# Performance work log

Hardware: AMD Instinct MI355X
Metric: run time of the kernel (lower is better)

The kernel has to match this reference:

```python
import jax, jax.numpy as jnp
import numpy as np

B, N = 64, 16384
EPS_RT = 1e-06  # recovery_time epsilon from the torch code


def _init_params(key):
    ks = jax.random.split(key, 10)
    s = 0.1
    p = {}
    # ContextEncoder: 4 -> 16 -> 8 -> 1 (hidden_dim=8, first layer hidden*2)
    p['ctx_W1'] = jax.random.normal(ks[0], (4, 16), jnp.float32) * s
    p['ctx_b1'] = jnp.zeros((16,), jnp.float32)
    p['ctx_W2'] = jax.random.normal(ks[1], (16, 8), jnp.float32) * s
    p['ctx_b2'] = jnp.zeros((8,), jnp.float32)
    p['ctx_W3'] = jax.random.normal(ks[2], (8, 1), jnp.float32) * s
    p['ctx_b3'] = jnp.zeros((1,), jnp.float32)
    # RiskPropagationNetwork: 4 -> 64 -> 32 -> 16 -> 1
    p['p_W1'] = jax.random.normal(ks[3], (4, 64), jnp.float32) * s
    p['p_b1'] = jnp.zeros((64,), jnp.float32)
    p['p_W2'] = jax.random.normal(ks[4], (64, 32), jnp.float32) * s
    p['p_b2'] = jnp.zeros((32,), jnp.float32)
    p['p_W3'] = jax.random.normal(ks[5], (32, 16), jnp.float32) * s
    p['p_b3'] = jnp.zeros((16,), jnp.float32)
    p['p_Wo'] = jax.random.normal(ks[6], (16, 1), jnp.float32) * s
    p['p_bo'] = jnp.zeros((1,), jnp.float32)
    # learned scalar risk-component weights
    p['w_threat'] = jnp.float32(0.4)
    p['w_impact'] = jnp.float32(0.3)
    p['w_vuln'] = jnp.float32(0.2)
    p['w_ctx'] = jnp.float32(0.1)
    return p


def setup_inputs() -> dict:
    key = jax.random.key(0)
    ks = jax.random.split(key, 12)
    inp = {
        'threat_predictions': jax.random.normal(ks[0], (B, N), jnp.float32),
        'criticality': jax.random.uniform(ks[1], (B, N), jnp.float32),
        'connectivity': jax.random.uniform(ks[2], (B, N), jnp.float32),
        'sensitivity': jax.random.uniform(ks[3], (B, N), jnp.float32),
        'business_value': jax.random.uniform(ks[4], (B, N), jnp.float32),
        'data_sensitivity': jax.random.uniform(ks[5], (B, N), jnp.float32),
        'compliance_requirements': jax.random.uniform(ks[6], (B, N), jnp.float32),
        'recovery_time': jax.random.uniform(ks[7], (B, N), jnp.float32),
        'severity': jax.random.uniform(ks[8], (B, N), jnp.float32) * 10.0,
    }
    inp.update(_init_params(ks[9]))
    return inp


def _forward(threat_predictions, criticality, connectivity, sensitivity,
             business_value, data_sensitivity, compliance_requirements,
             recovery_time, severity,
             ctx_W1, ctx_b1, ctx_W2, ctx_b2, ctx_W3, ctx_b3,
             p_W1, p_b1, p_W2, p_b2, p_W3, p_b3, p_Wo, p_bo,
             w_threat, w_impact, w_vuln, w_ctx):
    # --- risk components ---
    threat_risk = jax.nn.sigmoid(threat_predictions * 3.0)
    m = jnp.max(criticality)
    impact_risk = jnp.where(m > 0, criticality / jnp.maximum(m, 1e-12), criticality)
    vuln_risk = severity / 10.0
    # ContextEncoder: concat 4 context scalars -> MLP -> sigmoid
    ctx_in = jnp.stack([business_value, data_sensitivity, compliance_requirements,
                        1.0 / (recovery_time + EPS_RT)], axis=-1)  # [B,N,4]
    h = jax.nn.relu(ctx_in @ ctx_W1 + ctx_b1)
    h = jax.nn.relu(h @ ctx_W2 + ctx_b2)
    context_risk = jax.nn.sigmoid((h @ ctx_W3 + ctx_b3)[..., 0])
    # --- weighted combination with normalized learned weights ---
    total_w = w_threat + w_impact + w_vuln + w_ctx
    base_risk = (w_threat * threat_risk + w_impact * impact_risk
                 + w_vuln * vuln_risk + w_ctx * context_risk) / total_w
    # --- RiskPropagationNetwork (dropout is identity in eval) ---
    feats = jnp.stack([base_risk, criticality, connectivity, sensitivity], axis=-1)  # [B,N,4]
    x = jax.nn.relu(feats @ p_W1 + p_b1)
    x = jax.nn.relu(x @ p_W2 + p_b2)
    x = jax.nn.relu(x @ p_W3 + p_b3)
    return jax.nn.sigmoid((x @ p_Wo + p_bo)[..., 0])  # [B,N]


def reference(threat_predictions, criticality, connectivity, sensitivity,
              business_value, data_sensitivity, compliance_requirements,
              recovery_time, severity,
              ctx_W1, ctx_b1, ctx_W2, ctx_b2, ctx_W3, ctx_b3,
              p_W1, p_b1, p_W2, p_b2, p_W3, p_b3, p_Wo, p_bo,
              w_threat, w_impact, w_vuln, w_ctx):
    return _forward(threat_predictions, criticality, connectivity, sensitivity,
                    business_value, data_sensitivity, compliance_requirements,
                    recovery_time, severity,
                    ctx_W1, ctx_b1, ctx_W2, ctx_b2, ctx_W3, ctx_b3,
                    p_W1, p_b1, p_W2, p_b2, p_W3, p_b3, p_Wo, p_bo,
                    w_threat, w_impact, w_vuln, w_ctx)
```

## Files before the change

### kernel.cpp

```cpp
#include <hip/hip_runtime.h>
#include <hip/hip_bf16.h>

typedef short bf16x8 __attribute__((ext_vector_type(8)));
typedef float f32x4 __attribute__((ext_vector_type(4)));
typedef unsigned int uint;

#define TOTAL (64 * 16384)
#define ITERS 2
#define BLOCKS (TOTAL / (256 * ITERS))
#define MAXBLOCKS 256

__device__ __forceinline__ uint bf16rne(float x) {
    uint b = __float_as_uint(x);
    return (b + 0x7fffu + ((b >> 16) & 1u)) >> 16;
}
__device__ __forceinline__ short bf16s(float x) { return (short)bf16rne(x); }
__device__ __forceinline__ uint pk2(float lo, float hi) {
    __hip_bfloat162 h2 = __float22bfloat162_rn(make_float2(lo, hi));
    uint u;
    __builtin_memcpy(&u, &h2, sizeof(u));
    return u;
}
__device__ __forceinline__ float relu_(float x) { return fmaxf(x, 0.0f); }
__device__ __forceinline__ float fast_sigmoid(float x) {
    return __builtin_amdgcn_rcpf(1.0f + __expf(-x));
}
__device__ __forceinline__ float dot4r(f32x4 v, float4 w) {
    return fmaf(relu_(v[0]), w.x, fmaf(relu_(v[1]), w.y,
           fmaf(relu_(v[2]), w.z, relu_(v[3]) * w.w)));
}
__device__ __forceinline__ bf16x8 u4bf(uint4 u) {
    bf16x8 r;
    __builtin_memcpy(&r, &u, sizeof(r));
    return r;
}

__global__ __launch_bounds__(256) void crit_max_kernel(
        const float* __restrict__ crit, float* __restrict__ ws, int n4) {
    __shared__ float smax[4];
    const int tid = threadIdx.x;
    float m = 0.0f;
    const float4* c4 = (const float4*)crit;
    for (int i = blockIdx.x * 256 + tid; i < n4; i += gridDim.x * 256) {
        float4 v = c4[i];
        m = fmaxf(fmaxf(m, v.x), fmaxf(fmaxf(v.y, v.z), v.w));
    }
#pragma unroll
    for (int off = 32; off > 0; off >>= 1)
        m = fmaxf(m, __shfl_xor(m, off));
    if ((tid & 63) == 0) smax[tid >> 6] = m;
    __syncthreads();
    if (tid == 0)
        ws[blockIdx.x] = fmaxf(fmaxf(smax[0], smax[1]), fmaxf(smax[2], smax[3]));
}

__global__ __launch_bounds__(256, 3) void risk_mfma_kernel(
        const float* __restrict__ tp,   const float* __restrict__ crit,
        const float* __restrict__ conn, const float* __restrict__ sens,
        const float* __restrict__ bv,   const float* __restrict__ dsv,
        const float* __restrict__ comp, const float* __restrict__ rt,
        const float* __restrict__ sev,
        const float* __restrict__ ctxW1, const float* __restrict__ ctxb1,
        const float* __restrict__ ctxW2, const float* __restrict__ ctxb2,
        const float* __restrict__ ctxW3, const float* __restrict__ ctxb3,
        const float* __restrict__ pW1,  const float* __restrict__ pb1,
        const float* __restrict__ pW2,  const float* __restrict__ pb2,
        const float* __restrict__ pW3,  const float* __restrict__ pb3,
        const float* __restrict__ pWo,  const float* __restrict__ pbo,
        const float* __restrict__ w_threat, const float* __restrict__ w_impact,
        const float* __restrict__ w_vuln,   const float* __restrict__ w_ctx,
        const float* __restrict__ ws_part,
        float* __restrict__ out) {
    const int lane = threadIdx.x & 63;
    const int g    = lane >> 4;
    const int c    = lane & 15;

    const bf16x8 z8 = {0,0,0,0,0,0,0,0};
    const f32x4  z4 = {0.f,0.f,0.f,0.f};

    float m;
    {
        float4 pm4 = ((const float4*)ws_part)[lane];
        float pm = fmaxf(fmaxf(pm4.x, pm4.y), fmaxf(pm4.z, pm4.w));
#pragma unroll
        for (int off = 32; off > 0; off >>= 1)
            pm = fmaxf(pm, __shfl_xor(pm, off));
        m = pm;
    }

    const float wt  = w_threat[0], wi = w_impact[0], wv = w_vuln[0], wc = w_ctx[0];
    const float inv_tw = 1.0f / (wt + wi + wv + wc);
    const float imul = (m > 0.0f) ? 1.0f / fmaxf(m, 1e-12f) : 1.0f;
    const float wcn = wc * inv_tw;
    const float cb3 = ctxb3[0];
    const float pbo0 = pbo[0];

    bf16x8 cwAll = z8;
    cwAll[0] = bf16s(ctxW1[c]);
    cwAll[1] = bf16s(ctxW1[16 + c]);
    cwAll[2] = bf16s(ctxW1[32 + c]);
    cwAll[3] = bf16s(ctxW1[48 + c]);
    cwAll[4] = bf16s(ctxb1[c]);
    bf16x8 cw2All = z8;
    if (c < 8) {
#pragma unroll
        for (int i = 0; i < 4; ++i)
            cw2All[i] = bf16s(ctxW2[(4 * g + i) * 8 + c]);
    }
    bf16x8 w1All[4];
#pragma unroll
    for (int nt = 0; nt < 4; ++nt) {
        bf16x8 f = z8;
        f[0] = bf16s(pW1[nt * 16 + c]);
        f[4] = bf16s(pb1[nt * 16 + c]);
        f[5] = bf16s(pW1[64 + nt * 16 + c]);
        f[6] = bf16s(pW1[128 + nt * 16 + c]);
        f[7] = bf16s(pW1[192 + nt * 16 + c]);
        w1All[nt] = f;
    }
    bf16x8 w2A[2][2];
#pragma unroll
    for (int mt = 0; mt < 2; ++mt)
#pragma unroll
        for (int kf = 0; kf < 2; ++kf) {
            bf16x8 f;
#pragma unroll
            for (int i = 0; i < 4; ++i)
                f[i] = bf16s(pW2[(kf * 32 + 4 * g + i) * 32 + mt * 16 + c]);
#pragma unroll
            for (int i = 4; i < 8; ++i)
                f[i] = bf16s(pW2[(kf * 32 + 16 + 4 * g + (i - 4)) * 32 + mt * 16 + c]);
            w2A[mt][kf] = f;
        }
    bf16x8 w3A;
#pragma unroll
    for (int i = 0; i < 4; ++i) w3A[i] = bf16s(pW3[(4 * g + i) * 16 + c]);
#pragma unroll
    for (int i = 4; i < 8; ++i) w3A[i] = bf16s(pW3[(16 + 4 * g + (i - 4)) * 16 + c]);

    f32x4 b2i[2];
#pragma unroll
    for (int mt = 0; mt < 2; ++mt) {
        float4 t = ((const float4*)pb2)[mt * 4 + g];
        b2i[mt] = (f32x4){t.x, t.y, t.z, t.w};
    }
    float4 t3 = ((const float4*)pb3)[g];
    f32x4 b3i = (f32x4){t3.x, t3.y, t3.z, t3.w};
    f32x4 cb2i = z4;
    float4 cw3v = make_float4(0.f, 0.f, 0.f, 0.f);
    if (g < 2) {
        float4 tb = ((const float4*)ctxb2)[g];
        cb2i = (f32x4){tb.x, tb.y, tb.z, tb.w};
        cw3v = ((const float4*)ctxW3)[g];
    }
    float4 wog = ((const float4*)pWo)[g];

    const int eblock = blockIdx.x * (256 * ITERS);

#pragma unroll 1
    for (int it = 0; it < ITERS; ++it) {
        const int ewave = eblock + it * 256 + (int)(threadIdx.x >> 6) * 64;
        uint4 fv;
        float pbase;
        {
            const int e = ewave + lane;
            float tpv = tp[e], cv = crit[e], cnv = conn[e], snv = sens[e];
            float bvv = bv[e], dvv = dsv[e], cpv = comp[e], rtv = rt[e], svv = sev[e];
            float threat = fast_sigmoid(3.0f * tpv);
            float impact = cv * imul;
            float vuln   = svv * 0.1f;
            float invrt  = __builtin_amdgcn_rcpf(rtv + 1e-6f);
            pbase = (wt * threat + wi * impact + wv * vuln) * inv_tw;
            fv.x = pk2(bvv, dvv);
            fv.y = pk2(cpv, invrt);
            fv.z = pk2(1.0f, cv);
            fv.w = pk2(cnv, snv);
        }
        uint4 Bt[4];
#pragma unroll
        for (int t = 0; t < 4; ++t) {
            bool sel = (g == t);
            Bt[t].x = sel ? fv.x : 0u;
            Bt[t].y = sel ? fv.y : 0u;
            Bt[t].z = sel ? fv.z : 0u;
            Bt[t].w = sel ? fv.w : 0u;
        }
        float pcv[4];
#pragma unroll
        for (int t = 0; t < 4; ++t) {
            f32x4 cc1 = __builtin_amdgcn_mfma_f32_16x16x32_bf16(cwAll, u4bf(Bt[t]), z4, 0, 0, 0);
            uint4 bu;
            bu.x = pk2(relu_(cc1[0]), relu_(cc1[1]));
            bu.y = pk2(relu_(cc1[2]), relu_(cc1[3]));
            bu.z = 0u;
            bu.w = 0u;
            f32x4 cc2 = __builtin_amdgcn_mfma_f32_16x16x32_bf16(cw2All, u4bf(bu), cb2i, 0, 0, 0);
            pcv[t] = dot4r(cc2, cw3v);
        }
#pragma unroll
        for (int t = 0; t < 4; ++t) {
            pcv[t] += __shfl_xor(pcv[t], 16);
            pcv[t] += __shfl_xor(pcv[t], 32);
        }
        float pcsel = (g == 0) ? pcv[0] : (g == 1) ? pcv[1] : (g == 2) ? pcv[2] : pcv[3];
        float ctxr  = fast_sigmoid(pcsel + cb3);
        float base  = fmaf(wcn, ctxr, pbase);
        uint  bb    = bf16rne(base);
        float pv[4];
#pragma unroll
        for (int t = 0; t < 4; ++t) {
            uint4 pB;
            pB.x = (g == t) ? bb : 0u;
            pB.y = Bt[t].y;
            pB.z = Bt[t].z;
            pB.w = Bt[t].w;
            bf16x8 bp = u4bf(pB);
            uint l1p[4][2];
#pragma unroll
            for (int nt = 0; nt < 4; ++nt) {
                f32x4 c1 = __builtin_amdgcn_mfma_f32_16x16x32_bf16(w1All[nt], bp, z4, 0, 0, 0);
                l1p[nt][0] = pk2(relu_(c1[0]), relu_(c1[1]));
                l1p[nt][1] = pk2(relu_(c1[2]), relu_(c1[3]));
            }
            uint4 B0 = make_uint4(l1p[0][0], l1p[0][1], l1p[1][0], l1p[1][1]);
            uint4 B1 = make_uint4(l1p[2][0], l1p[2][1], l1p[3][0], l1p[3][1]);
            bf16x8 b0 = u4bf(B0), b1 = u4bf(B1);
            uint l2p[2][2];
#pragma unroll
            for (int mt = 0; mt < 2; ++mt) {
                f32x4 acc = __builtin_amdgcn_mfma_f32_16x16x32_bf16(w2A[mt][0], b0, b2i[mt], 0, 0, 0);
                f32x4 c2  = __builtin_amdgcn_mfma_f32_16x16x32_bf16(w2A[mt][1], b1, acc, 0, 0, 0);
                l2p[mt][0] = pk2(relu_(c2[0]), relu_(c2[1]));
                l2p[mt][1] = pk2(relu_(c2[2]), relu_(c2[3]));
            }
            uint4 B3 = make_uint4(l2p[0][0], l2p[0][1], l2p[1][0], l2p[1][1]);
            f32x4 c3 = __builtin_amdgcn_mfma_f32_16x16x32_bf16(w3A, u4bf(B3), b3i, 0, 0, 0);
            pv[t] = dot4r(c3, wog);
        }
#pragma unroll
        for (int t = 0; t < 4; ++t) {
            pv[t] += __shfl_xor(pv[t], 16);
            pv[t] += __shfl_xor(pv[t], 32);
        }
        float psel = (g == 0) ? pv[0] : (g == 1) ? pv[1] : (g == 2) ? pv[2] : pv[3];
        out[ewave + lane] = fast_sigmoid(psel + pbo0);
    }
}

extern "C" void kernel_launch(void* const* d_in, const int* in_sizes, int n_in,
                              void* d_out, int out_size, void* d_ws, size_t ws_size,
                              hipStream_t stream) {
    const float* tp    = (const float*)d_in[0];
    const float* crit  = (const float*)d_in[1];
    const float* conn  = (const float*)d_in[2];
    const float* sens  = (const float*)d_in[3];
    const float* bv    = (const float*)d_in[4];
    const float* dsv   = (const float*)d_in[5];
    const float* comp  = (const float*)d_in[6];
    const float* rt    = (const float*)d_in[7];
    const float* sev   = (const float*)d_in[8];
    const float* ctxW1 = (const float*)d_in[9];
    const float* ctxb1 = (const float*)d_in[10];
    const float* ctxW2 = (const float*)d_in[11];
    const float* ctxb2 = (const float*)d_in[12];
    const float* ctxW3 = (const float*)d_in[13];
    const float* ctxb3 = (const float*)d_in[14];
    const float* pW1   = (const float*)d_in[15];
    const float* pb1   = (const float*)d_in[16];
    const float* pW2   = (const float*)d_in[17];
    const float* pb2   = (const float*)d_in[18];
    const float* pW3   = (const float*)d_in[19];
    const float* pb3   = (const float*)d_in[20];
    const float* pWo   = (const float*)d_in[21];
    const float* pbo   = (const float*)d_in[22];
    const float* w_t   = (const float*)d_in[23];
    const float* w_i   = (const float*)d_in[24];
    const float* w_v   = (const float*)d_in[25];
    const float* w_c   = (const float*)d_in[26];

    float* ws_part = (float*)d_ws;
    float* out = (float*)d_out;

    crit_max_kernel<<<MAXBLOCKS, 256, 0, stream>>>(crit, ws_part, TOTAL / 4);
    risk_mfma_kernel<<<BLOCKS, 256, 0, stream>>>(
        tp, crit, conn, sens, bv, dsv, comp, rt, sev,
        ctxW1, ctxb1, ctxW2, ctxb2, ctxW3, ctxb3,
        pW1, pb1, pW2, pb2, pW3, pb3, pWo, pbo,
        w_t, w_i, w_v, w_c, ws_part, out);
}
```

Measured before the change: 39.34 us.

## Precompute MFMA weight fragments in prep kernel and drop per-block iteration loop

Adds a single-wave prep kernel that reduces the criticality partial maxima, normalizes the scalar weights, and packs all bf16 MFMA weight fragments and biases into the workspace. The main kernel then loads the prepacked fragments with vector loads instead of doing scattered scalar loads and bf16 conversions in every block. The per-block ITERS loop is removed, so each block handles 256 elements and the grid doubles. The cost is an extra tiny kernel launch on the critical path, and the per-block setup is now paid once per 256 elements instead of once per 512.

```diff
diff --git a/kernel.cpp b/kernel.cpp
--- a/kernel.cpp
+++ b/kernel.cpp
@@ -6,9 +6,12 @@
 typedef unsigned int uint;
 
 #define TOTAL (64 * 16384)
-#define ITERS 2
-#define BLOCKS (TOTAL / (256 * ITERS))
+#define BLOCKS (TOTAL / 256)
 #define MAXBLOCKS 256
+
+#define WS_PART(ws) ((float*)(ws))
+#define WS_SCAL(ws) ((float*)((char*)(ws) + 2048))
+#define WS_FRAG(ws) ((uint4*)((char*)(ws) + 4096))
 
 __device__ __forceinline__ uint bf16rne(float x) {
     uint b = __float_as_uint(x);
@@ -34,9 +37,19 @@
     __builtin_memcpy(&r, &u, sizeof(r));
     return r;
 }
+__device__ __forceinline__ uint4 bfu4(bf16x8 f) {
+    uint4 u;
+    __builtin_memcpy(&u, &f, sizeof(u));
+    return u;
+}
+__device__ __forceinline__ uint4 f4u4(float4 f) {
+    uint4 u;
+    __builtin_memcpy(&u, &f, sizeof(u));
+    return u;
+}
 
 __global__ __launch_bounds__(256) void crit_max_kernel(
-        const float* __restrict__ crit, float* __restrict__ ws, int n4) {
+        const float* __restrict__ crit, float* __restrict__ part, int n4) {
     __shared__ float smax[4];
     const int tid = threadIdx.x;
     float m = 0.0f;
@@ -51,15 +64,10 @@
     if ((tid & 63) == 0) smax[tid >> 6] = m;
     __syncthreads();
     if (tid == 0)
-        ws[blockIdx.x] = fmaxf(fmaxf(smax[0], smax[1]), fmaxf(smax[2], smax[3]));
-}
-
-__global__ __launch_bounds__(256, 3) void risk_mfma_kernel(
-        const float* __restrict__ tp,   const float* __restrict__ crit,
-        const float* __restrict__ conn, const float* __restrict__ sens,
-        const float* __restrict__ bv,   const float* __restrict__ dsv,
-        const float* __restrict__ comp, const float* __restrict__ rt,
-        const float* __restrict__ sev,
+        part[blockIdx.x] = fmaxf(fmaxf(smax[0], smax[1]), fmaxf(smax[2], smax[3]));
+}
+
+__global__ __launch_bounds__(64) void prep_kernel(
         const float* __restrict__ ctxW1, const float* __restrict__ ctxb1,
         const float* __restrict__ ctxW2, const float* __restrict__ ctxb2,
         const float* __restrict__ ctxW3, const float* __restrict__ ctxb3,
@@ -69,45 +77,53 @@
         const float* __restrict__ pWo,  const float* __restrict__ pbo,
         const float* __restrict__ w_threat, const float* __restrict__ w_impact,
         const float* __restrict__ w_vuln,   const float* __restrict__ w_ctx,
-        const float* __restrict__ ws_part,
-        float* __restrict__ out) {
-    const int lane = threadIdx.x & 63;
+        void* __restrict__ ws) {
+    const int lane = threadIdx.x;
     const int g    = lane >> 4;
     const int c    = lane & 15;
-
     const bf16x8 z8 = {0,0,0,0,0,0,0,0};
-    const f32x4  z4 = {0.f,0.f,0.f,0.f};
-
-    float m;
-    {
-        float4 pm4 = ((const float4*)ws_part)[lane];
+
+    {
+        const float* part = WS_PART(ws);
+        float4 pm4 = ((const float4*)part)[lane];
         float pm = fmaxf(fmaxf(pm4.x, pm4.y), fmaxf(pm4.z, pm4.w));
 #pragma unroll
         for (int off = 32; off > 0; off >>= 1)
             pm = fmaxf(pm, __shfl_xor(pm, off));
-        m = pm;
-    }
-
-    const float wt  = w_threat[0], wi = w_impact[0], wv = w_vuln[0], wc = w_ctx[0];
-    const float inv_tw = 1.0f / (wt + wi + wv + wc);
-    const float imul = (m > 0.0f) ? 1.0f / fmaxf(m, 1e-12f) : 1.0f;
-    const float wcn = wc * inv_tw;
-    const float cb3 = ctxb3[0];
-    const float pbo0 = pbo[0];
-
-    bf16x8 cwAll = z8;
-    cwAll[0] = bf16s(ctxW1[c]);
-    cwAll[1] = bf16s(ctxW1[16 + c]);
-    cwAll[2] = bf16s(ctxW1[32 + c]);
-    cwAll[3] = bf16s(ctxW1[48 + c]);
-    cwAll[4] = bf16s(ctxb1[c]);
-    bf16x8 cw2All = z8;
-    if (c < 8) {
-#pragma unroll
-        for (int i = 0; i < 4; ++i)
-            cw2All[i] = bf16s(ctxW2[(4 * g + i) * 8 + c]);
-    }
-    bf16x8 w1All[4];
+        if (lane == 0) {
+            float wt = w_threat[0], wi = w_impact[0], wv = w_vuln[0], wc = w_ctx[0];
+            float inv_tw = 1.0f / (wt + wi + wv + wc);
+            float* scal = WS_SCAL(ws);
+            scal[0] = wt * inv_tw;
+            scal[1] = wi * inv_tw;
+            scal[2] = wv * inv_tw;
+            scal[3] = wc * inv_tw;
+            scal[4] = (pm > 0.0f) ? 1.0f / fmaxf(pm, 1e-12f) : 1.0f;
+            scal[5] = ctxb3[0];
+            scal[6] = pbo[0];
+            scal[7] = 0.0f;
+        }
+    }
+
+    uint4* fr = WS_FRAG(ws);
+    {
+        bf16x8 f = z8;
+        f[0] = bf16s(ctxW1[c]);
+        f[1] = bf16s(ctxW1[16 + c]);
+        f[2] = bf16s(ctxW1[32 + c]);
+        f[3] = bf16s(ctxW1[48 + c]);
+        f[4] = bf16s(ctxb1[c]);
+        fr[0 * 64 + lane] = bfu4(f);
+    }
+    {
+        bf16x8 f = z8;
+        if (c < 8) {
+#pragma unroll
+            for (int i = 0; i < 4; ++i)
+                f[i] = bf16s(ctxW2[(4 * g + i) * 8 + c]);
+        }
+        fr[1 * 64 + lane] = bfu4(f);
+    }
 #pragma unroll
     for (int nt = 0; nt < 4; ++nt) {
         bf16x8 f = z8;
@@ -116,9 +132,8 @@
         f[5] = bf16s(pW1[64 + nt * 16 + c]);
         f[6] = bf16s(pW1[128 + nt * 16 + c]);
         f[7] = bf16s(pW1[192 + nt * 16 + c]);
-        w1All[nt] = f;
-    }
-    bf16x8 w2A[2][2];
+        fr[(2 + nt) * 64 + lane] = bfu4(f);
+    }
 #pragma unroll
     for (int mt = 0; mt < 2; ++mt)
 #pragma unroll
@@ -130,121 +145,149 @@
 #pragma unroll
             for (int i = 4; i < 8; ++i)
                 f[i] = bf16s(pW2[(kf * 32 + 16 + 4 * g + (i - 4)) * 32 + mt * 16 + c]);
-            w2A[mt][kf] = f;
-        }
-    bf16x8 w3A;
-#pragma unroll
-    for (int i = 0; i < 4; ++i) w3A[i] = bf16s(pW3[(4 * g + i) * 16 + c]);
-#pragma unroll
-    for (int i = 4; i < 8; ++i) w3A[i] = bf16s(pW3[(16 + 4 * g + (i - 4)) * 16 + c]);
-
-    f32x4 b2i[2];
-#pragma unroll
-    for (int mt = 0; mt < 2; ++mt) {
-        float4 t = ((const float4*)pb2)[mt * 4 + g];
-        b2i[mt] = (f32x4){t.x, t.y, t.z, t.w};
-    }
-    float4 t3 = ((const float4*)pb3)[g];
-    f32x4 b3i = (f32x4){t3.x, t3.y, t3.z, t3.w};
-    f32x4 cb2i = z4;
-    float4 cw3v = make_float4(0.f, 0.f, 0.f, 0.f);
-    if (g < 2) {
-        float4 tb = ((const float4*)ctxb2)[g];
-        cb2i = (f32x4){tb.x, tb.y, tb.z, tb.w};
-        cw3v = ((const float4*)ctxW3)[g];
-    }
-    float4 wog = ((const float4*)pWo)[g];
-
-    const int eblock = blockIdx.x * (256 * ITERS);
-
-#pragma unroll 1
-    for (int it = 0; it < ITERS; ++it) {
-        const int ewave = eblock + it * 256 + (int)(threadIdx.x >> 6) * 64;
-        uint4 fv;
-        float pbase;
-        {
-            const int e = ewave + lane;
-            float tpv = tp[e], cv = crit[e], cnv = conn[e], snv = sens[e];
-            float bvv = bv[e], dvv = dsv[e], cpv = comp[e], rtv = rt[e], svv = sev[e];
-            float threat = fast_sigmoid(3.0f * tpv);
-            float impact = cv * imul;
-            float vuln   = svv * 0.1f;
-            float invrt  = __builtin_amdgcn_rcpf(rtv + 1e-6f);
-            pbase = (wt * threat + wi * impact + wv * vuln) * inv_tw;
-            fv.x = pk2(bvv, dvv);
-            fv.y = pk2(cpv, invrt);
-            fv.z = pk2(1.0f, cv);
-            fv.w = pk2(cnv, snv);
-        }
-        uint4 Bt[4];
-#pragma unroll
-        for (int t = 0; t < 4; ++t) {
-            bool sel = (g == t);
-            Bt[t].x = sel ? fv.x : 0u;
-            Bt[t].y = sel ? fv.y : 0u;
-            Bt[t].z = sel ? fv.z : 0u;
-            Bt[t].w = sel ? fv.w : 0u;
-        }
-        float pcv[4];
-#pragma unroll
-        for (int t = 0; t < 4; ++t) {
-            f32x4 cc1 = __builtin_amdgcn_mfma_f32_16x16x32_bf16(cwAll, u4bf(Bt[t]), z4, 0, 0, 0);
-            uint4 bu;
-            bu.x = pk2(relu_(cc1[0]), relu_(cc1[1]));
-            bu.y = pk2(relu_(cc1[2]), relu_(cc1[3]));
-            bu.z = 0u;
-            bu.w = 0u;
-            f32x4 cc2 = __builtin_amdgcn_mfma_f32_16x16x32_bf16(cw2All, u4bf(bu), cb2i, 0, 0, 0);
-            pcv[t] = dot4r(cc2, cw3v);
-        }
-#pragma unroll
-        for (int t = 0; t < 4; ++t) {
-            pcv[t] += __shfl_xor(pcv[t], 16);
-            pcv[t] += __shfl_xor(pcv[t], 32);
-        }
-        float pcsel = (g == 0) ? pcv[0] : (g == 1) ? pcv[1] : (g == 2) ? pcv[2] : pcv[3];
-        float ctxr  = fast_sigmoid(pcsel + cb3);
-        float base  = fmaf(wcn, ctxr, pbase);
-        uint  bb    = bf16rne(base);
-        float pv[4];
-#pragma unroll
-        for (int t = 0; t < 4; ++t) {
-            uint4 pB;
-            pB.x = (g == t) ? bb : 0u;
-            pB.y = Bt[t].y;
-            pB.z = Bt[t].z;
-            pB.w = Bt[t].w;
-            bf16x8 bp = u4bf(pB);
-            uint l1p[4][2];
-#pragma unroll
-            for (int nt = 0; nt < 4; ++nt) {
-                f32x4 c1 = __builtin_amdgcn_mfma_f32_16x16x32_bf16(w1All[nt], bp, z4, 0, 0, 0);
-                l1p[nt][0] = pk2(relu_(c1[0]), relu_(c1[1]));
-                l1p[nt][1] = pk2(relu_(c1[2]), relu_(c1[3]));
-            }
-            uint4 B0 = make_uint4(l1p[0][0], l1p[0][1], l1p[1][0], l1p[1][1]);
-            uint4 B1 = make_uint4(l1p[2][0], l1p[2][1], l1p[3][0], l1p[3][1]);
-            bf16x8 b0 = u4bf(B0), b1 = u4bf(B1);
-            uint l2p[2][2];
-#pragma unroll
-            for (int mt = 0; mt < 2; ++mt) {
-                f32x4 acc = __builtin_amdgcn_mfma_f32_16x16x32_bf16(w2A[mt][0], b0, b2i[mt], 0, 0, 0);
-                f32x4 c2  = __builtin_amdgcn_mfma_f32_16x16x32_bf16(w2A[mt][1], b1, acc, 0, 0, 0);
-                l2p[mt][0] = pk2(relu_(c2[0]), relu_(c2[1]));
-                l2p[mt][1] = pk2(relu_(c2[2]), relu_(c2[3]));
-            }
-            uint4 B3 = make_uint4(l2p[0][0], l2p[0][1], l2p[1][0], l2p[1][1]);
-            f32x4 c3 = __builtin_amdgcn_mfma_f32_16x16x32_bf16(w3A, u4bf(B3), b3i, 0, 0, 0);
-            pv[t] = dot4r(c3, wog);
-        }
-#pragma unroll
-        for (int t = 0; t < 4; ++t) {
-            pv[t] += __shfl_xor(pv[t], 16);
-            pv[t] += __shfl_xor(pv[t], 32);
-        }
-        float psel = (g == 0) ? pv[0] : (g == 1) ? pv[1] : (g == 2) ? pv[2] : pv[3];
-        out[ewave + lane] = fast_sigmoid(psel + pbo0);
-    }
+            fr[(6 + mt * 2 + kf) * 64 + lane] = bfu4(f);
+        }
+    {
+        bf16x8 f;
+#pragma unroll
+        for (int i = 0; i < 4; ++i) f[i] = bf16s(pW3[(4 * g + i) * 16 + c]);
+#pragma unroll
+        for (int i = 4; i < 8; ++i) f[i] = bf16s(pW3[(16 + 4 * g + (i - 4)) * 16 + c]);
+        fr[10 * 64 + lane] = bfu4(f);
+    }
+    fr[11 * 64 + lane] = f4u4(((const float4*)pb2)[g]);
+    fr[12 * 64 + lane] = f4u4(((const float4*)pb2)[4 + g]);
+    fr[13 * 64 + lane] = f4u4(((const float4*)pb3)[g]);
+    float4 zf = make_float4(0.f, 0.f, 0.f, 0.f);
+    fr[14 * 64 + lane] = f4u4((g < 2) ? ((const float4*)ctxb2)[g] : zf);
+    fr[15 * 64 + lane] = f4u4((g < 2) ? ((const float4*)ctxW3)[g] : zf);
+    fr[16 * 64 + lane] = f4u4(((const float4*)pWo)[g]);
+}
+
+__global__ __launch_bounds__(256, 3) void risk_mfma_kernel(
+        const float* __restrict__ tp,   const float* __restrict__ crit,
+        const float* __restrict__ conn, const float* __restrict__ sens,
+        const float* __restrict__ bv,   const float* __restrict__ dsv,
+        const float* __restrict__ comp, const float* __restrict__ rt,
+        const float* __restrict__ sev,
+        const void* __restrict__ ws,
+        float* __restrict__ out) {
+    const int lane = threadIdx.x & 63;
+    const int g    = lane >> 4;
+    const f32x4 z4 = {0.f,0.f,0.f,0.f};
+
+    const float* scal = WS_SCAL(ws);
+    const float wtn = scal[0], win = scal[1], wvn = scal[2], wcn = scal[3];
+    const float imul = scal[4], cb3 = scal[5], pbo0 = scal[6];
+
+    const uint4* fr = WS_FRAG(ws);
+    bf16x8 cwAll  = u4bf(fr[0 * 64 + lane]);
+    bf16x8 cw2All = u4bf(fr[1 * 64 + lane]);
+    bf16x8 w1All[4];
+#pragma unroll
+    for (int nt = 0; nt < 4; ++nt) w1All[nt] = u4bf(fr[(2 + nt) * 64 + lane]);
+    bf16x8 w2A[2][2];
+#pragma unroll
+    for (int mt = 0; mt < 2; ++mt)
+#pragma unroll
+        for (int kf = 0; kf < 2; ++kf)
+            w2A[mt][kf] = u4bf(fr[(6 + mt * 2 + kf) * 64 + lane]);
+    bf16x8 w3A = u4bf(fr[10 * 64 + lane]);
+    f32x4 b2i[2], b3i, cb2i;
+    float4 cw3v, wog;
+    __builtin_memcpy(&b2i[0], &fr[11 * 64 + lane], 16);
+    __builtin_memcpy(&b2i[1], &fr[12 * 64 + lane], 16);
+    __builtin_memcpy(&b3i,    &fr[13 * 64 + lane], 16);
+    __builtin_memcpy(&cb2i,   &fr[14 * 64 + lane], 16);
+    __builtin_memcpy(&cw3v,   &fr[15 * 64 + lane], 16);
+    __builtin_memcpy(&wog,    &fr[16 * 64 + lane], 16);
+
+    const int ewave = blockIdx.x * 256 + (int)(threadIdx.x >> 6) * 64;
+
+    uint4 fv;
+    float pbase;
+    {
+        const int e = ewave + lane;
+        float tpv = tp[e], cv = crit[e], cnv = conn[e], snv = sens[e];
+        float bvv = bv[e], dvv = dsv[e], cpv = comp[e], rtv = rt[e], svv = sev[e];
+        float threat = fast_sigmoid(3.0f * tpv);
+        float impact = cv * imul;
+        float vuln   = svv * 0.1f;
+        float invrt  = __builtin_amdgcn_rcpf(rtv + 1e-6f);
+        pbase = fmaf(wtn, threat, fmaf(win, impact, wvn * vuln));
+        fv.x = pk2(bvv, dvv);
+        fv.y = pk2(cpv, invrt);
+        fv.z = pk2(1.0f, cv);
+        fv.w = pk2(cnv, snv);
+    }
+    uint4 Bt[4];
+#pragma unroll
+    for (int t = 0; t < 4; ++t) {
+        bool sel = (g == t);
+        Bt[t].x = sel ? fv.x : 0u;
+        Bt[t].y = sel ? fv.y : 0u;
+        Bt[t].z = sel ? fv.z : 0u;
+        Bt[t].w = sel ? fv.w : 0u;
+    }
+    float pcv[4];
+#pragma unroll
+    for (int t = 0; t < 4; ++t) {
+        f32x4 cc1 = __builtin_amdgcn_mfma_f32_16x16x32_bf16(cwAll, u4bf(Bt[t]), z4, 0, 0, 0);
+        uint4 bu;
+        bu.x = pk2(relu_(cc1[0]), relu_(cc1[1]));
+        bu.y = pk2(relu_(cc1[2]), relu_(cc1[3]));
+        bu.z = 0u;
+        bu.w = 0u;
+        f32x4 cc2 = __builtin_amdgcn_mfma_f32_16x16x32_bf16(cw2All, u4bf(bu), cb2i, 0, 0, 0);
+        pcv[t] = dot4r(cc2, cw3v);
+    }
+#pragma unroll
+    for (int t = 0; t < 4; ++t) {
+        pcv[t] += __shfl_xor(pcv[t], 16);
+        pcv[t] += __shfl_xor(pcv[t], 32);
+    }
+    float pcsel = (g == 0) ? pcv[0] : (g == 1) ? pcv[1] : (g == 2) ? pcv[2] : pcv[3];
+    float ctxr  = fast_sigmoid(pcsel + cb3);
+    float base  = fmaf(wcn, ctxr, pbase);
+    uint  bb    = bf16rne(base);
+    float pv[4];
+#pragma unroll
+    for (int t = 0; t < 4; ++t) {
+        uint4 pB;
+        pB.x = (g == t) ? bb : 0u;
+        pB.y = Bt[t].y;
+        pB.z = Bt[t].z;
+        pB.w = Bt[t].w;
+        bf16x8 bp = u4bf(pB);
+        uint l1p[4][2];
+#pragma unroll
+        for (int nt = 0; nt < 4; ++nt) {
+            f32x4 c1 = __builtin_amdgcn_mfma_f32_16x16x32_bf16(w1All[nt], bp, z4, 0, 0, 0);
+            l1p[nt][0] = pk2(relu_(c1[0]), relu_(c1[1]));
+            l1p[nt][1] = pk2(relu_(c1[2]), relu_(c1[3]));
+        }
+        uint4 B0 = make_uint4(l1p[0][0], l1p[0][1], l1p[1][0], l1p[1][1]);
+        uint4 B1 = make_uint4(l1p[2][0], l1p[2][1], l1p[3][0], l1p[3][1]);
+        bf16x8 b0 = u4bf(B0), b1 = u4bf(B1);
+        uint l2p[2][2];
+#pragma unroll
+        for (int mt = 0; mt < 2; ++mt) {
+            f32x4 acc = __builtin_amdgcn_mfma_f32_16x16x32_bf16(w2A[mt][0], b0, b2i[mt], 0, 0, 0);
+            f32x4 c2  = __builtin_amdgcn_mfma_f32_16x16x32_bf16(w2A[mt][1], b1, acc, 0, 0, 0);
+            l2p[mt][0] = pk2(relu_(c2[0]), relu_(c2[1]));
+            l2p[mt][1] = pk2(relu_(c2[2]), relu_(c2[3]));
+        }
+        uint4 B3 = make_uint4(l2p[0][0], l2p[0][1], l2p[1][0], l2p[1][1]);
+        f32x4 c3 = __builtin_amdgcn_mfma_f32_16x16x32_bf16(w3A, u4bf(B3), b3i, 0, 0, 0);
+        pv[t] = dot4r(c3, wog);
+    }
+#pragma unroll
+    for (int t = 0; t < 4; ++t) {
+        pv[t] += __shfl_xor(pv[t], 16);
+        pv[t] += __shfl_xor(pv[t], 32);
+    }
+    float psel = (g == 0) ? pv[0] : (g == 1) ? pv[1] : (g == 2) ? pv[2] : pv[3];
+    out[ewave + lane] = fast_sigmoid(psel + pbo0);
 }
 
 extern "C" void kernel_launch(void* const* d_in, const int* in_sizes, int n_in,
@@ -278,13 +321,13 @@
     const float* w_v   = (const float*)d_in[25];
     const float* w_c   = (const float*)d_in[26];
 
-    float* ws_part = (float*)d_ws;
     float* out = (float*)d_out;
 
-    crit_max_kernel<<<MAXBLOCKS, 256, 0, stream>>>(crit, ws_part, TOTAL / 4);
-    risk_mfma_kernel<<<BLOCKS, 256, 0, stream>>>(
-        tp, crit, conn, sens, bv, dsv, comp, rt, sev,
+    crit_max_kernel<<<MAXBLOCKS, 256, 0, stream>>>(crit, WS_PART(d_ws), TOTAL / 4);
+    prep_kernel<<<1, 64, 0, stream>>>(
         ctxW1, ctxb1, ctxW2, ctxb2, ctxW3, ctxb3,
         pW1, pb1, pW2, pb2, pW3, pb3, pWo, pbo,
-        w_t, w_i, w_v, w_c, ws_part, out);
-}
+        w_t, w_i, w_v, w_c, d_ws);
+    risk_mfma_kernel<<<BLOCKS, 256, 0, stream>>>(
+        tp, crit, conn, sens, bv, dsv, comp, rt, sev, d_ws, out);
+}
```

Result: faster. 37.51 us (-4.7%).
